# Performance work log

Measured on AMD Instinct MI355X. Metric: run time of the kernel, lower is better.

Reference implementation:

```python
import jax, jax.numpy as jnp
import numpy as np

B, T, N, D, H = 4, 8, 128, 256, 8
DH = D // H
SH_HID = 16
NUM_FEATS = 3
NUM_COEFF = 4  # l=0 (1) + l=1 (3)
Y0_CONST = 0.28209479177387814   # 1/(2*sqrt(pi)), e3nn 'integral' norm
Y1_CONST = 0.4886025119029199    # sqrt(3/(4*pi))


def setup_inputs() -> dict:
    key = jax.random.key(0)
    ks = jax.random.split(key, 16)
    rn = lambda k, shape, s=1.0: jax.random.normal(k, shape, dtype=jnp.float32) * s
    return {
        "x_0": rn(ks[0], (B, T, N, D)),
        "v_0": rn(ks[1], (B, T, N, D)),
        "concatenated_features": rn(ks[2], (B, T, N, D)),
        "q_data": rn(ks[3], (B, T, N, D)),
        "mask": jnp.ones((B, 1, N, 1), dtype=bool),
        "Wq": rn(ks[4], (D, D), 0.02), "bq": jnp.zeros((D,), jnp.float32),
        "Wkv": rn(ks[5], (NUM_FEATS, D, 2 * D), 0.02),
        "bkv": jnp.zeros((NUM_FEATS, 2 * D), jnp.float32),
        "Wo": rn(ks[6], (D, D), 0.02), "bo": jnp.zeros((D,), jnp.float32),
        "feature_weights": rn(ks[7], (NUM_FEATS,), 0.1),
        "attention_denom": jnp.full((H,), float(DH), dtype=jnp.float32),
        "sh_W1": rn(ks[8], (NUM_COEFF, SH_HID), 0.3), "sh_b1": jnp.zeros((SH_HID,), jnp.float32),
        "sh_W2": rn(ks[9], (SH_HID, SH_HID), 0.3), "sh_b2": jnp.zeros((SH_HID,), jnp.float32),
        "sh_W3": rn(ks[10], (SH_HID, H), 0.3), "sh_b3": jnp.zeros((H,), jnp.float32),
    }


def _rope(t, mask, T_, N_):
    # t: [B,H,S,dh]; time-only RoPE, groups of N_ nodes share a timestep. offset=0.
    B_, H_, S, dh = t.shape
    half = dh // 2
    freqs = 1.0 / (1000.0 ** (2.0 * jnp.arange(half, dtype=jnp.float32) / dh))  # [half]
    pos = jnp.repeat(jnp.arange(T_, dtype=jnp.float32), N_)  # [S]
    angle = pos[:, None] * freqs[None, :]  # [S, half]
    mask_seq = jnp.broadcast_to(mask, (B_, T_, N_, 1)).reshape(B_, 1, S, 1)
    cos_t = jnp.where(mask_seq, jnp.cos(angle)[None, None], 1.0)  # [B,1,S,half]
    sin_t = jnp.where(mask_seq, jnp.sin(angle)[None, None], 0.0)
    t1, t2 = t[..., 0::2], t[..., 1::2]
    return jnp.stack([t1 * cos_t - t2 * sin_t, t1 * sin_t + t2 * cos_t], axis=-1).reshape(t.shape)


def _sh_bias(coords, W1, b1, W2, b2, W3, b3):
    # coords: [B,S,3] -> bias [B,H,S,S]
    rel = coords[:, :, None, :] - coords[:, None, :, :]  # [B,S,S,3]
    norm = jnp.sqrt(jnp.sum(rel * rel, axis=-1, keepdims=True))
    u = rel / (norm + 1e-6)
    Y0 = jnp.full(u.shape[:-1] + (1,), Y0_CONST, dtype=u.dtype)
    Y1 = Y1_CONST * u[..., jnp.array([1, 2, 0])]  # e3nn l=1 order (y,z,x)
    sh = jnp.concatenate([Y0, Y1], axis=-1)  # [B,S,S,4]
    h = jax.nn.silu(sh @ W1 + b1)
    h = jax.nn.silu(h @ W2 + b2)
    bias = h @ W3 + b3  # [B,S,S,H]
    return jnp.transpose(bias, (0, 3, 1, 2))


def reference(x_0, v_0, concatenated_features, q_data, mask,
              Wq, bq, Wkv, bkv, Wo, bo, feature_weights, attention_denom,
              sh_W1, sh_b1, sh_W2, sh_b2, sh_W3, sh_b3):
    B_, T_, N_, D_ = q_data.shape
    S = T_ * N_
    H_ = attention_denom.shape[0]
    dh = D_ // H_

    q = (q_data.reshape(B_, S, D_) @ Wq + bq).reshape(B_, S, H_, dh).transpose(0, 2, 1, 3)
    q = _rope(q, mask, T_, N_)

    coords = x_0[..., :3].reshape(B_, S, 3)
    bias = _sh_bias(coords, sh_W1, sh_b1, sh_W2, sh_b2, sh_W3, sh_b3)  # [B,H,S,S]

    key_mask = jnp.broadcast_to(mask, (B_, T_, N_, 1)).reshape(B_, 1, 1, S)
    gates = jax.nn.softmax(feature_weights)

    out_sum = jnp.zeros_like(q)
    for i, feat in enumerate((x_0, v_0, concatenated_features)):
        kv = feat.reshape(B_, S, D_) @ Wkv[i] + bkv[i]  # [B,S,2D]
        k = kv[..., :D_].reshape(B_, S, H_, dh).transpose(0, 2, 1, 3)
        v = kv[..., D_:].reshape(B_, S, H_, dh).transpose(0, 2, 1, 3)
        k = _rope(k, mask, T_, N_)
        scores = jnp.einsum('bhqd,bhkd->bhqk', q, k) / attention_denom[None, :, None, None]
        scores = scores + bias
        scores = jnp.where(key_mask, scores, -1e9)
        attn = jax.nn.softmax(scores, axis=-1)
        out_sum = out_sum + gates[i] * jnp.einsum('bhqk,bhkd->bhqd', attn, v)

    out = out_sum.transpose(0, 2, 1, 3).reshape(B_, S, D_) @ Wo + bo  # [B,S,D]
    return out.reshape(B_ * T_, N_, D_)
```

## Files before the change

### kernel.cpp

```cpp
#include <hip/hip_runtime.h>
#include <hip/hip_bf16.h>
#include <math.h>


typedef __bf16 bf16;
typedef __attribute__((ext_vector_type(8))) __bf16 bf16x8;
typedef __attribute__((ext_vector_type(4))) __bf16 bf16x4;
typedef __attribute__((ext_vector_type(4))) float  f32x4;

#define MFMA16(a,b,c) __builtin_amdgcn_mfma_f32_16x16x32_bf16((a),(b),(c),0,0,0)
#define FRCP(x) __builtin_amdgcn_rcpf(x)

__global__ __launch_bounds__(256) void proj_kernel(
    const float* __restrict__ x0, const float* __restrict__ v0,
    const float* __restrict__ cf, const float* __restrict__ qd,
    const float* __restrict__ Wq, const float* __restrict__ bq,
    const float* __restrict__ Wkv, const float* __restrict__ bkv,
    const float* __restrict__ dn,
    bf16* __restrict__ Qb, bf16* __restrict__ Kb, bf16* __restrict__ Vtb)
{
  const int mtc = blockIdx.x;
  const int znt = blockIdx.y;
  int z, nt;
  if (znt < 4){ z = 0; nt = znt; } else { z = 1 + ((znt-4)>>3); nt = (znt-4)&7; }

  const float* A; const float* W; const float* bias; int ldw;
  if (z == 0){ A = qd; W = Wq; bias = bq; ldw = 256; }
  else {
    A = (z==1) ? x0 : (z==2) ? v0 : cf;
    W = Wkv + (size_t)(z-1)*256*512;
    bias = bkv + (size_t)(z-1)*512;
    ldw = 512;
  }

  __shared__ alignas(16) bf16 lds_w[64*264];
  __shared__ alignas(16) bf16 ostg[4][1152];
  const int t  = threadIdx.x;
  const int n0 = nt*64;

  {
    int c4 = t & 15, kr = t >> 4;
    #pragma unroll
    for (int i=0;i<16;i++){
      int k = kr + i*16;
      float4 v = *(const float4*)(W + (size_t)k*ldw + n0 + c4*4);
      lds_w[(c4*4+0)*264 + k] = (bf16)v.x;
      lds_w[(c4*4+1)*264 + k] = (bf16)v.y;
      lds_w[(c4*4+2)*264 + k] = (bf16)v.z;
      lds_w[(c4*4+3)*264 + k] = (bf16)v.w;
    }
  }
  __syncthreads();

  const int w = t>>6, lane = t&63, lrow = lane&15, g = lane>>4;
  const f32x4 zf = {0.f,0.f,0.f,0.f};
  const bool isV = (z>0) && (nt>=4);

  const float Cln = 0.43172239f;
  const float fr_e = __expf(-Cln * (float)(lrow>>1));
  const float fr_o = __expf(-Cln * (float)(8 + (lrow>>1)));
  float rs0 = 1.f, rs1 = 1.f;
  if (z==0){ rs0 = 1.f/dn[(nt*2)&7]; rs1 = 1.f/dn[(nt*2+1)&7]; }

  for (int mi=0; mi<4; mi++){
    const int mt = mtc*4 + mi;
    const float* Arow = A + (size_t)(mt*64 + w*16 + lrow)*256;

    f32x4 acc[4] = {zf,zf,zf,zf};
    #pragma unroll
    for (int ks=0;ks<8;ks++){
      float4 a0 = *(const float4*)(Arow + ks*32 + g*8);
      float4 a1 = *(const float4*)(Arow + ks*32 + g*8 + 4);
      bf16x8 af = {(bf16)a0.x,(bf16)a0.y,(bf16)a0.z,(bf16)a0.w,
                   (bf16)a1.x,(bf16)a1.y,(bf16)a1.z,(bf16)a1.w};
      #pragma unroll
      for (int n4=0;n4<4;n4++){
        bf16x8 bb = *(const bf16x8*)(lds_w + (n4*16+lrow)*264 + ks*32 + g*8);
        acc[n4] = MFMA16(af, bb, acc[n4]);
      }
    }

    if (!isV){
      const float tpos = (float)((mt>>1)&7);
      float ae = tpos*fr_e, ao = tpos*fr_o;
      float cs_e = __cosf(ae), sn_e = __sinf(ae);
      float cs_o = __cosf(ao), sn_o = __sinf(ao);
      #pragma unroll
      for (int n4=0;n4<4;n4++){
        int gcol = n0 + n4*16 + lrow;
        float bv = bias[gcol];
        float cs = (n4&1)? cs_o : cs_e;
        float sn = (n4&1)? sn_o : sn_e;
        float rs = (n4>>1)? rs1 : rs0;
        #pragma unroll
        for (int rr=0;rr<4;rr++){
          float v = acc[n4][rr] + bv;
          float p = __shfl_xor(v, 1);
          float o = (lrow&1) ? (p*sn + v*cs) : (v*cs - p*sn);
          o *= rs;
          ostg[w][(g*4+rr)*72 + n4*16 + lrow] = (bf16)o;
        }
      }
      asm volatile("s_waitcnt lgkmcnt(0)" ::: "memory");
      int row = lane>>2, c8 = lane&3;
      int srow = mt*64 + w*16 + row;
      int bb = srow>>10, s = srow&1023;
      #pragma unroll
      for (int hh=0; hh<2; hh++){
        bf16x8 val = *(const bf16x8*)(ostg[w] + row*72 + hh*32 + c8*8);
        int h = (nt*2 + hh)&7;
        bf16* dst = (z==0) ? (Qb + ((size_t)(bb*8+h)*1024 + s)*32 + c8*8)
                           : (Kb + ((size_t)(((z-1)*4+bb)*8+h)*1024 + s)*32 + c8*8);
        *(bf16x8*)dst = val;
      }
    } else {
      #pragma unroll
      for (int n4=0;n4<4;n4++){
        int gcol = n0 + n4*16 + lrow;
        float bv = bias[gcol];
        int hd = gcol - 256; int h = hd>>5, d = hd&31;
        int grow0 = mt*64 + w*16 + g*4;
        int bb = grow0>>10, s0 = grow0&1023;
        int s0p = (s0 & ~31) | (((s0>>2)&3)<<3) | (((s0>>4)&1)<<2);
        bf16x4 pk;
        #pragma unroll
        for (int rr=0;rr<4;rr++) pk[rr] = (bf16)(acc[n4][rr] + bv);
        *(bf16x4*)(Vtb + (((size_t)((z-1)*4+bb)*8 + h)*32 + d)*1024 + s0p) = pk;
      }
    }
  }
}

__global__ __launch_bounds__(512, 2) void attn_kernel(
    const bf16* __restrict__ Qb, const bf16* __restrict__ Kb, const bf16* __restrict__ Vtb,
    const float* __restrict__ x0, const float* __restrict__ fw,
    const float* __restrict__ W1, const float* __restrict__ b1,
    const float* __restrict__ W2, const float* __restrict__ b2,
    const float* __restrict__ W3, const float* __restrict__ b3,
    float* __restrict__ osum)
{
  const int bid = blockIdx.x;
  const int xcd = bid & 7;
  const int b   = xcd >> 1;
  const int qt  = (xcd & 1)*32 + (bid >> 3);
  const int q0  = qt*16;
  const int t = threadIdx.x, w = t>>6, lane = t&63, lrow = lane&15, g = lane>>4;

  __shared__ float ckA[1024][3];
  __shared__ float biasT[2][8*64*17];

  bf16x8 w1f, w2f, w3f;
  #pragma unroll
  for (int j=0;j<8;j++){
    w1f[j] = (g==0 && j<4)   ? (bf16)W1[j*16 + lrow]       : (bf16)0.f;
    w2f[j] = (j<4)           ? (bf16)W2[(4*g+j)*16 + lrow] : (bf16)0.f;
    w3f[j] = (j<4 && lrow<8) ? (bf16)W3[(4*g+j)*8 + lrow]  : (bf16)0.f;
  }
  float b1r[4], b2r[4], b3r[4];
  #pragma unroll
  for (int rr=0;rr<4;rr++){
    b1r[rr] = b1[g*4+rr];
    b2r[rr] = b2[g*4+rr];
    b3r[rr] = (g<2) ? b3[g*4+rr] : 0.f;
  }

  float f0=fw[0], f1=fw[1], f2=fw[2];
  float fm = fmaxf(f0, fmaxf(f1,f2));
  float e0=__expf(f0-fm), e1=__expf(f1-fm), e2=__expf(f2-fm);
  float ei = FRCP(e0+e1+e2);
  float gate[3] = {e0*ei, e1*ei, e2*ei};

  bf16x8 qf = *(const bf16x8*)(Qb + (((size_t)(b*8+w)*1024) + q0 + lrow)*32 + g*8);

  #pragma unroll
  for (int u=0;u<2;u++){
    int key = u*512 + t;
    const float* src = x0 + ((size_t)b*1024 + key)*256;
    ckA[key][0] = src[0]; ckA[key][1] = src[1]; ckA[key][2] = src[2];
  }
  __syncthreads();
  const float cqx = ckA[q0+lrow][0], cqy = ckA[q0+lrow][1], cqz = ckA[q0+lrow][2];

  float l_run[3] = {0.f,0.f,0.f};
  const f32x4 zf = {0.f,0.f,0.f,0.f};
  f32x4 acc[3][2];
  #pragma unroll
  for (int i=0;i<3;i++){ acc[i][0] = zf; acc[i][1] = zf; }

  for (int kt=0;kt<16;kt++){
    const int k0 = kt*64;
    float* bT = biasT[kt&1];

    bf16x8 kpre[3][4], vpre[3][2][2];
    #pragma unroll
    for (int i=0;i<3;i++){
      const bf16* Kbase = Kb + ((size_t)(i*4+b)*8 + w)*1024*32;
      #pragma unroll
      for (int k16=0;k16<4;k16++)
        kpre[i][k16] = *(const bf16x8*)(Kbase + (size_t)(k0 + k16*16 + lrow)*32 + g*8);
      const bf16* Vbase = Vtb + ((size_t)(i*4+b)*8 + w)*32*1024;
      #pragma unroll
      for (int dt=0;dt<2;dt++){
        vpre[i][dt][0] = *(const bf16x8*)(Vbase + (size_t)(dt*16+lrow)*1024 + k0      + g*8);
        vpre[i][dt][1] = *(const bf16x8*)(Vbase + (size_t)(dt*16+lrow)*1024 + k0 + 32 + g*8);
      }
    }

    float ckx[8], cky[8], ckz[8];
    #pragma unroll
    for (int m8=0;m8<8;m8++){
      int m = w*8 + m8;
      ckx[m8] = ckA[k0+m][0]; cky[m8] = ckA[k0+m][1]; ckz[m8] = ckA[k0+m][2];
    }

    #pragma unroll
    for (int m8=0;m8<8;m8++){
      const int m = w*8 + m8;
      float rx = cqx - ckx[m8];
      float ry = cqy - cky[m8];
      float rz = cqz - ckz[m8];
      float inv = FRCP(__builtin_amdgcn_sqrtf(rx*rx+ry*ry+rz*rz) + 1e-6f);
      bf16x8 shf;
      #pragma unroll
      for (int j=0;j<8;j++) shf[j] = (bf16)0.f;
      if (g==0){
        shf[0] = (bf16)0.28209479177387814f;
        shf[1] = (bf16)(0.4886025119029199f*ry*inv);
        shf[2] = (bf16)(0.4886025119029199f*rz*inv);
        shf[3] = (bf16)(0.4886025119029199f*rx*inv);
      }
      f32x4 c1 = MFMA16(w1f, shf, zf);
      bf16x8 h1f;
      #pragma unroll
      for (int rr=0;rr<4;rr++){
        float hv = c1[rr] + b1r[rr];
        hv = hv * FRCP(1.f + __expf(-hv));
        bf16 hb = (bf16)hv;
        h1f[rr] = hb; h1f[rr+4] = hb;
      }
      f32x4 c2 = MFMA16(w2f, h1f, zf);
      bf16x8 h2f;
      #pragma unroll
      for (int rr=0;rr<4;rr++){
        float hv = c2[rr] + b2r[rr];
        hv = hv * FRCP(1.f + __expf(-hv));
        bf16 hb = (bf16)hv;
        h2f[rr] = hb; h2f[rr+4] = hb;
      }
      f32x4 c3 = MFMA16(w3f, h2f, zf);
      if (g < 2){
        #pragma unroll
        for (int rr=0;rr<4;rr++)
          bT[((g*4+rr)*64 + m)*17 + lrow] = c3[rr] + b3r[rr];
      }
    }
    __syncthreads();

    float bias_r[4][4];
    #pragma unroll
    for (int k16=0;k16<4;k16++)
      #pragma unroll
      for (int rr=0;rr<4;rr++)
        bias_r[k16][rr] = bT[(w*64 + k16*16 + g*4 + rr)*17 + lrow];

    #pragma unroll
    for (int i=0;i<3;i++){
      float p[4][4];
      float ls = 0.f;
      #pragma unroll
      for (int k16=0;k16<4;k16++){
        f32x4 sc = MFMA16(kpre[i][k16], qf, zf);
        #pragma unroll
        for (int rr=0;rr<4;rr++){
          float pv = __expf(sc[rr] + bias_r[k16][rr]);
          p[k16][rr] = pv;
          ls += pv;
        }
      }
      l_run[i] += ls;
      bf16x8 pf0, pf1;
      #pragma unroll
      for (int j=0;j<8;j++){
        pf0[j] = (bf16)p[(j>>2)][j&3];
        pf1[j] = (bf16)p[2+(j>>2)][j&3];
      }
      #pragma unroll
      for (int dt=0;dt<2;dt++){
        acc[i][dt] = MFMA16(vpre[i][dt][0], pf0, acc[i][dt]);
        acc[i][dt] = MFMA16(vpre[i][dt][1], pf1, acc[i][dt]);
      }
    }
  }

  float linv[3];
  #pragma unroll
  for (int i=0;i<3;i++){
    float l = l_run[i];
    l += __shfl_xor(l, 16);
    l += __shfl_xor(l, 32);
    linv[i] = gate[i]*FRCP(l);
  }
  #pragma unroll
  for (int dt=0;dt<2;dt++){
    f32x4 o;
    #pragma unroll
    for (int rr=0;rr<4;rr++)
      o[rr] = acc[0][dt][rr]*linv[0] + acc[1][dt][rr]*linv[1] + acc[2][dt][rr]*linv[2];
    *(f32x4*)(osum + ((size_t)b*1024 + q0 + lrow)*256 + w*32 + dt*16 + g*4) = o;
  }
}

__global__ __launch_bounds__(256) void oproj_kernel(
    const float* __restrict__ As, const float* __restrict__ Wo,
    const float* __restrict__ bo, float* __restrict__ out)
{
  const int mt = blockIdx.x, nt = blockIdx.y;
  __shared__ alignas(16) bf16 lds_a[64*264];
  __shared__ alignas(16) bf16 lds_w[64*264];
  const int t = threadIdx.x;
  const int n0 = nt*64;
  #pragma unroll
  for (int i=0;i<16;i++){
    int flat = i*256 + t;
    int r = flat >> 6, c4 = flat & 63;
    float4 v = *(const float4*)(As + (size_t)(mt*64 + r)*256 + c4*4);
    bf16* dst = lds_a + r*264 + c4*4;
    dst[0]=(bf16)v.x; dst[1]=(bf16)v.y; dst[2]=(bf16)v.z; dst[3]=(bf16)v.w;
  }
  {
    int c4 = t & 15, kr = t >> 4;
    #pragma unroll
    for (int i=0;i<16;i++){
      int k = kr + i*16;
      float4 v = *(const float4*)(Wo + (size_t)k*256 + n0 + c4*4);
      lds_w[(c4*4+0)*264 + k] = (bf16)v.x;
      lds_w[(c4*4+1)*264 + k] = (bf16)v.y;
      lds_w[(c4*4+2)*264 + k] = (bf16)v.z;
      lds_w[(c4*4+3)*264 + k] = (bf16)v.w;
    }
  }
  __syncthreads();
  const int w = t>>6, lane = t&63, lrow = lane&15, g = lane>>4;
  const f32x4 zf = {0.f,0.f,0.f,0.f};
  f32x4 acc[4] = {zf,zf,zf,zf};
  #pragma unroll
  for (int ks=0;ks<8;ks++){
    bf16x8 a = *(const bf16x8*)(lds_a + (w*16+lrow)*264 + ks*32 + g*8);
    #pragma unroll
    for (int n4=0;n4<4;n4++){
      bf16x8 bb = *(const bf16x8*)(lds_w + (n4*16+lrow)*264 + ks*32 + g*8);
      acc[n4] = MFMA16(a, bb, acc[n4]);
    }
  }
  #pragma unroll
  for (int n4=0;n4<4;n4++){
    int gcol = n0 + n4*16 + lrow;
    float bv = bo[gcol];
    #pragma unroll
    for (int rr=0;rr<4;rr++){
      int grow = mt*64 + w*16 + g*4 + rr;
      out[(size_t)grow*256 + gcol] = acc[n4][rr] + bv;
    }
  }
}

extern "C" void kernel_launch(void* const* d_in, const int* in_sizes, int n_in,
                              void* d_out, int out_size, void* d_ws, size_t ws_size,
                              hipStream_t stream)
{
  (void)in_sizes; (void)n_in; (void)out_size; (void)ws_size;
  const float* x0 = (const float*)d_in[0];
  const float* v0 = (const float*)d_in[1];
  const float* cf = (const float*)d_in[2];
  const float* qd = (const float*)d_in[3];
  const float* Wq = (const float*)d_in[5];
  const float* bq = (const float*)d_in[6];
  const float* Wkv= (const float*)d_in[7];
  const float* bkv= (const float*)d_in[8];
  const float* Wo = (const float*)d_in[9];
  const float* bo = (const float*)d_in[10];
  const float* fw = (const float*)d_in[11];
  const float* dn = (const float*)d_in[12];
  const float* W1 = (const float*)d_in[13];
  const float* b1 = (const float*)d_in[14];
  const float* W2 = (const float*)d_in[15];
  const float* b2 = (const float*)d_in[16];
  const float* W3 = (const float*)d_in[17];
  const float* b3 = (const float*)d_in[18];

  const size_t nQ = (size_t)4*8*1024*32;
  const size_t nK = (size_t)3*4*8*1024*32;
  bf16*  Qb   = (bf16*)d_ws;
  bf16*  Kb   = Qb + nQ;
  bf16*  Vtb  = Kb + nK;
  float* osum = (float*)(Vtb + nK);
  float* outp = (float*)d_out;

  hipLaunchKernelGGL(proj_kernel, dim3(16,28), dim3(256), 0, stream,
                     x0, v0, cf, qd, Wq, bq, Wkv, bkv, dn, Qb, Kb, Vtb);
  hipLaunchKernelGGL(attn_kernel, dim3(256), dim3(512), 0, stream,
                     Qb, Kb, Vtb, x0, fw, W1,b1,W2,b2,W3,b3, osum);
  hipLaunchKernelGGL(oproj_kernel, dim3(64,4), dim3(256), 0, stream,
                     osum, Wo, bo, outp);
}
```

Measured before the change: 228.1 us.

## Fuse output projection into attention kernel and software-pipeline bias MLP

Removes the separate output-projection kernel: each attention block transposes its 16x256 result into LDS as packed bf16 and multiplies it by Wo directly, writing the final output. This drops the osum round trip through global memory and one launch. The bias MLP for the next key tile is now computed while the current tile's attention math runs, using double-buffered LDS with one barrier per iteration. It also splits the row-sum reduction into a tree. In exchange, every block rereads Wo from global memory with scalar strided loads, which may cost more than the standalone GEMM did.

```diff
diff --git a/kernel.cpp b/kernel.cpp
--- a/kernel.cpp
+++ b/kernel.cpp
@@ -10,6 +10,13 @@
 
 #define MFMA16(a,b,c) __builtin_amdgcn_mfma_f32_16x16x32_bf16((a),(b),(c),0,0,0)
 #define FRCP(x) __builtin_amdgcn_rcpf(x)
+
+__device__ __forceinline__ unsigned pk2(float a, float b){
+  bf16 x = (bf16)a, y = (bf16)b;
+  unsigned short ux = __builtin_bit_cast(unsigned short, x);
+  unsigned short uy = __builtin_bit_cast(unsigned short, y);
+  return (unsigned)ux | ((unsigned)uy << 16);
+}
 
 __global__ __launch_bounds__(256) void proj_kernel(
     const float* __restrict__ x0, const float* __restrict__ v0,
@@ -137,7 +144,8 @@
     const float* __restrict__ W1, const float* __restrict__ b1,
     const float* __restrict__ W2, const float* __restrict__ b2,
     const float* __restrict__ W3, const float* __restrict__ b3,
-    float* __restrict__ osum)
+    const float* __restrict__ Wo, const float* __restrict__ bo,
+    float* __restrict__ out)
 {
   const int bid = blockIdx.x;
   const int xcd = bid & 7;
@@ -146,8 +154,9 @@
   const int q0  = qt*16;
   const int t = threadIdx.x, w = t>>6, lane = t&63, lrow = lane&15, g = lane>>4;
 
-  __shared__ float ckA[1024][3];
-  __shared__ float biasT[2][8*64*17];
+  __shared__ float smem[20480];
+  float* ckA = smem;
+  float* biasT0 = smem + 3072;
 
   bf16x8 w1f, w2f, w3f;
   #pragma unroll
@@ -176,49 +185,21 @@
   for (int u=0;u<2;u++){
     int key = u*512 + t;
     const float* src = x0 + ((size_t)b*1024 + key)*256;
-    ckA[key][0] = src[0]; ckA[key][1] = src[1]; ckA[key][2] = src[2];
+    ckA[key*3+0] = src[0]; ckA[key*3+1] = src[1]; ckA[key*3+2] = src[2];
   }
   __syncthreads();
-  const float cqx = ckA[q0+lrow][0], cqy = ckA[q0+lrow][1], cqz = ckA[q0+lrow][2];
-
-  float l_run[3] = {0.f,0.f,0.f};
-  const f32x4 zf = {0.f,0.f,0.f,0.f};
-  f32x4 acc[3][2];
-  #pragma unroll
-  for (int i=0;i<3;i++){ acc[i][0] = zf; acc[i][1] = zf; }
-
-  for (int kt=0;kt<16;kt++){
-    const int k0 = kt*64;
-    float* bT = biasT[kt&1];
-
-    bf16x8 kpre[3][4], vpre[3][2][2];
-    #pragma unroll
-    for (int i=0;i<3;i++){
-      const bf16* Kbase = Kb + ((size_t)(i*4+b)*8 + w)*1024*32;
-      #pragma unroll
-      for (int k16=0;k16<4;k16++)
-        kpre[i][k16] = *(const bf16x8*)(Kbase + (size_t)(k0 + k16*16 + lrow)*32 + g*8);
-      const bf16* Vbase = Vtb + ((size_t)(i*4+b)*8 + w)*32*1024;
-      #pragma unroll
-      for (int dt=0;dt<2;dt++){
-        vpre[i][dt][0] = *(const bf16x8*)(Vbase + (size_t)(dt*16+lrow)*1024 + k0      + g*8);
-        vpre[i][dt][1] = *(const bf16x8*)(Vbase + (size_t)(dt*16+lrow)*1024 + k0 + 32 + g*8);
-      }
-    }
-
-    float ckx[8], cky[8], ckz[8];
-    #pragma unroll
-    for (int m8=0;m8<8;m8++){
-      int m = w*8 + m8;
-      ckx[m8] = ckA[k0+m][0]; cky[m8] = ckA[k0+m][1]; ckz[m8] = ckA[k0+m][2];
-    }
-
+  const float cqx = ckA[(q0+lrow)*3+0], cqy = ckA[(q0+lrow)*3+1], cqz = ckA[(q0+lrow)*3+2];
+
+  auto MLP = [&](int kt_){
+    const int k0 = kt_*64;
+    float* bT = biasT0 + (kt_&1)*8704;
+    const f32x4 zf = {0.f,0.f,0.f,0.f};
     #pragma unroll
     for (int m8=0;m8<8;m8++){
       const int m = w*8 + m8;
-      float rx = cqx - ckx[m8];
-      float ry = cqy - cky[m8];
-      float rz = cqz - ckz[m8];
+      float rx = cqx - ckA[(k0+m)*3+0];
+      float ry = cqy - ckA[(k0+m)*3+1];
+      float rz = cqz - ckA[(k0+m)*3+2];
       float inv = FRCP(__builtin_amdgcn_sqrtf(rx*rx+ry*ry+rz*rz) + 1e-6f);
       bf16x8 shf;
       #pragma unroll
@@ -254,30 +235,63 @@
           bT[((g*4+rr)*64 + m)*17 + lrow] = c3[rr] + b3r[rr];
       }
     }
-    __syncthreads();
-
+  };
+
+  float l_run[3] = {0.f,0.f,0.f};
+  const f32x4 zf = {0.f,0.f,0.f,0.f};
+  f32x4 acc[3][2];
+  #pragma unroll
+  for (int i=0;i<3;i++){ acc[i][0] = zf; acc[i][1] = zf; }
+
+  MLP(0);
+  __syncthreads();
+
+  for (int kt=0;kt<16;kt++){
+    const int k0 = kt*64;
+
+    bf16x8 kpre[3][4], vpre[3][2][2];
+    #pragma unroll
+    for (int i=0;i<3;i++){
+      const bf16* Kbase = Kb + ((size_t)(i*4+b)*8 + w)*1024*32;
+      #pragma unroll
+      for (int k16=0;k16<4;k16++)
+        kpre[i][k16] = *(const bf16x8*)(Kbase + (size_t)(k0 + k16*16 + lrow)*32 + g*8);
+      const bf16* Vbase = Vtb + ((size_t)(i*4+b)*8 + w)*32*1024;
+      #pragma unroll
+      for (int dt=0;dt<2;dt++){
+        vpre[i][dt][0] = *(const bf16x8*)(Vbase + (size_t)(dt*16+lrow)*1024 + k0      + g*8);
+        vpre[i][dt][1] = *(const bf16x8*)(Vbase + (size_t)(dt*16+lrow)*1024 + k0 + 32 + g*8);
+      }
+    }
+    __builtin_amdgcn_sched_barrier(0);
+
+    const float* bTr = biasT0 + (kt&1)*8704;
     float bias_r[4][4];
     #pragma unroll
     for (int k16=0;k16<4;k16++)
       #pragma unroll
       for (int rr=0;rr<4;rr++)
-        bias_r[k16][rr] = bT[(w*64 + k16*16 + g*4 + rr)*17 + lrow];
+        bias_r[k16][rr] = bTr[(w*64 + k16*16 + g*4 + rr)*17 + lrow];
+
+    if (kt < 15) MLP(kt+1);
 
     #pragma unroll
     for (int i=0;i<3;i++){
       float p[4][4];
-      float ls = 0.f;
+      float lp[4];
       #pragma unroll
       for (int k16=0;k16<4;k16++){
         f32x4 sc = MFMA16(kpre[i][k16], qf, zf);
+        float s0 = 0.f;
         #pragma unroll
         for (int rr=0;rr<4;rr++){
           float pv = __expf(sc[rr] + bias_r[k16][rr]);
           p[k16][rr] = pv;
-          ls += pv;
+          s0 += pv;
         }
-      }
-      l_run[i] += ls;
+        lp[k16] = s0;
+      }
+      l_run[i] += (lp[0]+lp[1]) + (lp[2]+lp[3]);
       bf16x8 pf0, pf1;
       #pragma unroll
       for (int j=0;j<8;j++){
@@ -290,6 +304,7 @@
         acc[i][dt] = MFMA16(vpre[i][dt][1], pf1, acc[i][dt]);
       }
     }
+    __syncthreads();
   }
 
   float linv[3];
@@ -300,66 +315,42 @@
     l += __shfl_xor(l, 32);
     linv[i] = gate[i]*FRCP(l);
   }
+  f32x4 o[2];
+  #pragma unroll
+  for (int dt=0;dt<2;dt++)
+    #pragma unroll
+    for (int rr=0;rr<4;rr++)
+      o[dt][rr] = acc[0][dt][rr]*linv[0] + acc[1][dt][rr]*linv[1] + acc[2][dt][rr]*linv[2];
+
+  unsigned* osTp = (unsigned*)smem;
   #pragma unroll
   for (int dt=0;dt<2;dt++){
-    f32x4 o;
-    #pragma unroll
-    for (int rr=0;rr<4;rr++)
-      o[rr] = acc[0][dt][rr]*linv[0] + acc[1][dt][rr]*linv[1] + acc[2][dt][rr]*linv[2];
-    *(f32x4*)(osum + ((size_t)b*1024 + q0 + lrow)*256 + w*32 + dt*16 + g*4) = o;
-  }
-}
-
-__global__ __launch_bounds__(256) void oproj_kernel(
-    const float* __restrict__ As, const float* __restrict__ Wo,
-    const float* __restrict__ bo, float* __restrict__ out)
-{
-  const int mt = blockIdx.x, nt = blockIdx.y;
-  __shared__ alignas(16) bf16 lds_a[64*264];
-  __shared__ alignas(16) bf16 lds_w[64*264];
-  const int t = threadIdx.x;
-  const int n0 = nt*64;
-  #pragma unroll
-  for (int i=0;i<16;i++){
-    int flat = i*256 + t;
-    int r = flat >> 6, c4 = flat & 63;
-    float4 v = *(const float4*)(As + (size_t)(mt*64 + r)*256 + c4*4);
-    bf16* dst = lds_a + r*264 + c4*4;
-    dst[0]=(bf16)v.x; dst[1]=(bf16)v.y; dst[2]=(bf16)v.z; dst[3]=(bf16)v.w;
-  }
-  {
-    int c4 = t & 15, kr = t >> 4;
-    #pragma unroll
-    for (int i=0;i<16;i++){
-      int k = kr + i*16;
-      float4 v = *(const float4*)(Wo + (size_t)k*256 + n0 + c4*4);
-      lds_w[(c4*4+0)*264 + k] = (bf16)v.x;
-      lds_w[(c4*4+1)*264 + k] = (bf16)v.y;
-      lds_w[(c4*4+2)*264 + k] = (bf16)v.z;
-      lds_w[(c4*4+3)*264 + k] = (bf16)v.w;
-    }
+    int pb = w*16 + dt*8 + g*2;
+    osTp[(pb+0)*17 + lrow] = pk2(o[dt][0], o[dt][1]);
+    osTp[(pb+1)*17 + lrow] = pk2(o[dt][2], o[dt][3]);
   }
   __syncthreads();
-  const int w = t>>6, lane = t&63, lrow = lane&15, g = lane>>4;
-  const f32x4 zf = {0.f,0.f,0.f,0.f};
-  f32x4 acc[4] = {zf,zf,zf,zf};
-  #pragma unroll
-  for (int ks=0;ks<8;ks++){
-    bf16x8 a = *(const bf16x8*)(lds_a + (w*16+lrow)*264 + ks*32 + g*8);
-    #pragma unroll
-    for (int n4=0;n4<4;n4++){
-      bf16x8 bb = *(const bf16x8*)(lds_w + (n4*16+lrow)*264 + ks*32 + g*8);
-      acc[n4] = MFMA16(a, bb, acc[n4]);
-    }
-  }
-  #pragma unroll
-  for (int n4=0;n4<4;n4++){
-    int gcol = n0 + n4*16 + lrow;
-    float bv = bo[gcol];
+
+  #pragma unroll
+  for (int nt2=0;nt2<2;nt2++){
+    const int n0 = w*32 + nt2*16;
+    f32x4 c = zf;
+    #pragma unroll
+    for (int kb=0;kb<8;kb++){
+      bf16x8 af;
+      #pragma unroll
+      for (int j=0;j<8;j++)
+        af[j] = (bf16)Wo[(size_t)(kb*32 + g*8 + j)*256 + n0 + lrow];
+      union { unsigned u[4]; bf16x8 v; } bu;
+      #pragma unroll
+      for (int jj=0;jj<4;jj++)
+        bu.u[jj] = osTp[(kb*16 + g*4 + jj)*17 + lrow];
+      c = MFMA16(af, bu.v, c);
+    }
     #pragma unroll
     for (int rr=0;rr<4;rr++){
-      int grow = mt*64 + w*16 + g*4 + rr;
-      out[(size_t)grow*256 + gcol] = acc[n4][rr] + bv;
+      int n = n0 + g*4 + rr;
+      out[(size_t)(b*1024 + q0 + lrow)*256 + n] = c[rr] + bo[n];
     }
   }
 }
@@ -393,13 +384,10 @@
   bf16*  Qb   = (bf16*)d_ws;
   bf16*  Kb   = Qb + nQ;
   bf16*  Vtb  = Kb + nK;
-  float* osum = (float*)(Vtb + nK);
   float* outp = (float*)d_out;
 
   hipLaunchKernelGGL(proj_kernel, dim3(16,28), dim3(256), 0, stream,
                      x0, v0, cf, qd, Wq, bq, Wkv, bkv, dn, Qb, Kb, Vtb);
   hipLaunchKernelGGL(attn_kernel, dim3(256), dim3(512), 0, stream,
-                     Qb, Kb, Vtb, x0, fw, W1,b1,W2,b2,W3,b3, osum);
-  hipLaunchKernelGGL(oproj_kernel, dim3(64,4), dim3(256), 0, stream,
-                     osum, Wo, bo, outp);
+                     Qb, Kb, Vtb, x0, fw, W1,b1,W2,b2,W3,b3, Wo, bo, outp);
 }
```

Result: slower. 235.9 us (+3.4%).
